# Performance work log

Measured on AMD Instinct MI355X. Metric: run time of the kernel, lower is better.

## Reference

```python
import jax, jax.numpy as jnp
import numpy as np

BATCH, SEQ, IN_DIM, HID = 256, 256, 128, 512
KMAX, MID, NCLS = 4, 256, 16  # maxout features, maxout/dense/highway width, output classes


def hard_sigmoid(x):
    return jnp.clip(0.2 * x + 0.5, 0.0, 1.0)


def setup_inputs() -> dict:
    key = jax.random.key(0)
    ks = jax.random.split(key, 20)
    s = 0.05
    d = {
        'x': jax.random.normal(ks[0], (BATCH, SEQ, IN_DIM), jnp.float32),
        'W_z': jax.random.normal(ks[1], (IN_DIM, HID), jnp.float32) * s,
        'W_r': jax.random.normal(ks[2], (IN_DIM, HID), jnp.float32) * s,
        'W_h': jax.random.normal(ks[3], (IN_DIM, HID), jnp.float32) * s,
        'U_z': jax.random.normal(ks[4], (HID, HID), jnp.float32) * s,
        'U_r': jax.random.normal(ks[5], (HID, HID), jnp.float32) * s,
        'U_h': jax.random.normal(ks[6], (HID, HID), jnp.float32) * s,
        'b_z': jax.random.normal(ks[7], (HID,), jnp.float32) * s,
        'b_r': jax.random.normal(ks[8], (HID,), jnp.float32) * s,
        'b_h': jax.random.normal(ks[9], (HID,), jnp.float32) * s,
        'mo_W': jax.random.normal(ks[10], (KMAX, HID, MID), jnp.float32) * s,
        'mo_b': jax.random.normal(ks[11], (KMAX, MID), jnp.float32) * s,
        'd1_W': jax.random.normal(ks[12], (MID, MID), jnp.float32) * s,
        'd1_b': jax.random.normal(ks[13], (MID,), jnp.float32) * s,
        'hw_W': jax.random.normal(ks[14], (MID, MID), jnp.float32) * s,
        'hw_b': jax.random.normal(ks[15], (MID,), jnp.float32) * s,
        'hw_Wc': jax.random.normal(ks[16], (MID, MID), jnp.float32) * s,
        'hw_bc': jax.random.normal(ks[17], (MID,), jnp.float32) * s,
        'd2_W': jax.random.normal(ks[18], (MID, NCLS), jnp.float32) * s,
        'd2_b': jax.random.normal(ks[19], (NCLS,), jnp.float32) * s,
    }
    return d


def reference(x, W_z, W_r, W_h, U_z, U_r, U_h, b_z, b_r, b_h,
              mo_W, mo_b, d1_W, d1_b, hw_W, hw_b, hw_Wc, hw_bc, d2_W, d2_b):
    # ---- Theano-convention GRU (reset applied before U_h matmul) ----
    # Precompute all input projections in one batched GEMM each: [B,S,H]
    xz = jnp.einsum('bsi,ih->bsh', x, W_z) + b_z
    xr = jnp.einsum('bsi,ih->bsh', x, W_r) + b_r
    xh = jnp.einsum('bsi,ih->bsh', x, W_h) + b_h

    def step(h, xs):
        xzt, xrt, xht = xs
        z = hard_sigmoid(xzt + h @ U_z)
        r = hard_sigmoid(xrt + h @ U_r)
        hh = jnp.tanh(xht + (r * h) @ U_h)
        h_new = z * h + (1.0 - z) * hh
        return h_new, None

    h0 = jnp.zeros((x.shape[0], U_z.shape[0]), x.dtype)
    # scan over time axis: move S to leading dim
    xs = (jnp.swapaxes(xz, 0, 1), jnp.swapaxes(xr, 0, 1), jnp.swapaxes(xh, 0, 1))
    h, _ = jax.lax.scan(step, h0, xs)

    # ---- Maxout dense ----
    h = jnp.max(jnp.einsum('bi,kio->bko', h, mo_W) + mo_b, axis=1)
    # ---- Dense (linear) ----
    h = h @ d1_W + d1_b
    # ---- Highway ----
    t = jax.nn.sigmoid(h @ hw_Wc + hw_bc)
    hh = jax.nn.relu(h @ hw_W + hw_b)
    h = t * hh + (1.0 - t) * h
    # ---- Dense + softmax ----
    logits = h @ d2_W + d2_b
    return jax.nn.softmax(logits, axis=-1)
```

## Files before the change

### kernel.cpp

```cpp
#include <hip/hip_runtime.h>
#include <hip/hip_bf16.h>
#include <math.h>

#define BATCH 256
#define SEQN  256
#define INDIM 128
#define HID   512
#define MID   256
#define NCLS  16

#define NG 8
#define RG 32
#define NS 16
#define SC 32

typedef _Float16 half8 __attribute__((ext_vector_type(8)));
typedef float    f32x4 __attribute__((ext_vector_type(4)));

__device__ __forceinline__ half8 cc_load16(const _Float16* p) {
    half8 r;
    asm volatile("global_load_dwordx4 %0, %1, off sc1" : "=&v"(r) : "v"(p));
    return r;
}
__device__ __forceinline__ void cc_wait() {
    asm volatile("s_waitcnt vmcnt(0)" ::: "memory");
    __builtin_amdgcn_sched_barrier(0);
}
__device__ __forceinline__ void cc_store16(_Float16* p, _Float16 v) {
    unsigned short u = __builtin_bit_cast(unsigned short, v);
    asm volatile("global_store_short %0, %1, off sc1" :: "v"(p), "v"(u) : "memory");
}

__global__ __launch_bounds__(256) void pack_wA(
    const float* __restrict__ Uz, const float* __restrict__ Ur,
    const float* __restrict__ Wz, const float* __restrict__ Wr,
    _Float16* __restrict__ out)
{
    int idx = blockIdx.x * 256 + threadIdx.x;
    int j = idx & 7, l = (idx >> 3) & 63;
    int fr = idx >> 9;
    int kt = fr % 20; int r2 = fr / 20;
    int nt4 = r2 & 3; int s = r2 >> 2;
    int k = kt * 32 + (l >> 4) * 8 + j;
    int col = s * SC + (nt4 & 1) * 16 + (l & 15);
    const float* U = (nt4 < 2) ? Uz : Ur;
    const float* W = (nt4 < 2) ? Wz : Wr;
    float v = (k < HID) ? U[k * HID + col] : W[(k - HID) * HID + col];
    out[idx] = (_Float16)v;
}

__global__ __launch_bounds__(256) void pack_wB(
    const float* __restrict__ Uh, const float* __restrict__ Wh,
    _Float16* __restrict__ out)
{
    int idx = blockIdx.x * 256 + threadIdx.x;
    int j = idx & 7, l = (idx >> 3) & 63;
    int fr = idx >> 9;
    int kt = fr % 20; int r2 = fr / 20;
    int nt2 = r2 & 1; int s = r2 >> 1;
    int k = kt * 32 + (l >> 4) * 8 + j;
    int col = s * SC + nt2 * 16 + (l & 15);
    float v = (k < HID) ? Uh[k * HID + col] : Wh[(k - HID) * HID + col];
    out[idx] = (_Float16)v;
}

__global__ __launch_bounds__(512) void gru_sync(
    const float* __restrict__ x, const _Float16* __restrict__ GWA,
    const _Float16* __restrict__ GWB,
    const float* __restrict__ bz, const float* __restrict__ br,
    const float* __restrict__ bh,
    _Float16* __restrict__ HF, _Float16* __restrict__ VF,
    unsigned int* __restrict__ cnt, float* __restrict__ hout)
{
    __shared__ _Float16 WA[4][20][64][8];
    __shared__ _Float16 WB[2][20][64][8];
    __shared__ float    HO[RG][SC];

    const int tid = threadIdx.x;
    const int w = tid >> 6, l = tid & 63;
    const int bid = blockIdx.x;
    const int g = bid & 7, s = bid >> 3;
    const int m = l & 15;
    const int crow0 = (l >> 4) * 4;

    const int mt  = w & 1;
    const int nt4 = w >> 1;
    const int nt2 = w >> 1;

    {
        const float4* srcA = (const float4*)&GWA[(size_t)s * (4 * 20 * 512)];
        float4* dstA = (float4*)&WA[0][0][0][0];
        for (int i = tid; i < 4 * 20 * 512 / 8; i += 512) dstA[i] = srcA[i];
        const float4* srcB = (const float4*)&GWB[(size_t)s * (2 * 20 * 512)];
        float4* dstB = (float4*)&WB[0][0][0][0];
        for (int i = tid; i < 2 * 20 * 512 / 8; i += 512) dstB[i] = srcB[i];
    }
    for (int i = tid; i < RG * SC; i += 512) ((float*)HO)[i] = 0.f;

    float biasA;
    {
        int col = s * SC + (nt4 & 1) * 16 + m;
        biasA = (nt4 < 2) ? bz[col] : br[col];
    }
    float biasB = 0.f;
    if (w < 4) biasB = bh[s * SC + nt2 * 16 + m];

    unsigned int* flag = &cnt[g * 32];
    __syncthreads();

    float zreg[4];

    for (int t = 0; t < SEQN; ++t) {
        half8 hfr[16];
        {
            const _Float16* hf = &HF[(size_t)(g * 2 + mt) * 16 * 512];
            #pragma unroll
            for (int kt = 0; kt < 16; ++kt)
                hfr[kt] = cc_load16(hf + kt * 512 + l * 8);
        }

        half8 xf[4];
        {
            const float* xp = &x[(((size_t)(g * RG + mt * 16 + m)) * SEQN + t) * INDIM + (l >> 4) * 8];
            #pragma unroll
            for (int kf = 0; kf < 4; ++kf) {
                float4 a0 = *(const float4*)(xp + kf * 32);
                float4 a1 = *(const float4*)(xp + kf * 32 + 4);
                half8 hx;
                hx[0] = (_Float16)a0.x; hx[1] = (_Float16)a0.y;
                hx[2] = (_Float16)a0.z; hx[3] = (_Float16)a0.w;
                hx[4] = (_Float16)a1.x; hx[5] = (_Float16)a1.y;
                hx[6] = (_Float16)a1.z; hx[7] = (_Float16)a1.w;
                xf[kf] = hx;
            }
        }
        cc_wait();

        {
            f32x4 acc = {0.f, 0.f, 0.f, 0.f};
            #pragma unroll
            for (int kt = 0; kt < 16; ++kt) {
                half8 bf = *(const half8*)&WA[nt4][kt][l][0];
                acc = __builtin_amdgcn_mfma_f32_16x16x32_f16(hfr[kt], bf, acc, 0, 0, 0);
            }
            #pragma unroll
            for (int kf = 0; kf < 4; ++kf) {
                half8 bf = *(const half8*)&WA[nt4][16 + kf][l][0];
                acc = __builtin_amdgcn_mfma_f32_16x16x32_f16(xf[kf], bf, acc, 0, 0, 0);
            }
            if (nt4 < 2) {
                #pragma unroll
                for (int ri = 0; ri < 4; ++ri) {
                    float pre = acc[ri] + biasA;
                    zreg[ri] = fminf(fmaxf(0.2f * pre + 0.5f, 0.f), 1.f);
                }
            } else {
                #pragma unroll
                for (int ri = 0; ri < 4; ++ri) {
                    float pre = acc[ri] + biasA;
                    float gr = fminf(fmaxf(0.2f * pre + 0.5f, 0.f), 1.f);
                    int rloc = mt * 16 + crow0 + ri;
                    int cs = (nt4 & 1) * 16 + m;
                    float vv = gr * HO[rloc][cs];
                    cc_store16(&VF[(((size_t)(g * 2 + mt) * 16 + s) * 64 +
                                    ((crow0 + ri) + 16 * (cs >> 3))) * 8 + (cs & 7)],
                               (_Float16)vv);
                }
            }
        }

        asm volatile("s_waitcnt vmcnt(0)" ::: "memory");
        __syncthreads();
        if (tid == 0) {
            __hip_atomic_fetch_add(flag, 1u, __ATOMIC_RELAXED, __HIP_MEMORY_SCOPE_AGENT);
            unsigned int tgt = (unsigned int)(2 * t + 1) * NS;
            while (__hip_atomic_load(flag, __ATOMIC_RELAXED, __HIP_MEMORY_SCOPE_AGENT) < tgt) {}
        }
        __syncthreads();

        if (w < 4) {
            half8 vfr[16];
            {
                const _Float16* vf = &VF[(size_t)(g * 2 + mt) * 16 * 512];
                #pragma unroll
                for (int kt = 0; kt < 16; ++kt)
                    vfr[kt] = cc_load16(vf + kt * 512 + l * 8);
            }
            cc_wait();

            f32x4 acc2 = {0.f, 0.f, 0.f, 0.f};
            #pragma unroll
            for (int kt = 0; kt < 16; ++kt) {
                half8 bf = *(const half8*)&WB[nt2][kt][l][0];
                acc2 = __builtin_amdgcn_mfma_f32_16x16x32_f16(vfr[kt], bf, acc2, 0, 0, 0);
            }
            #pragma unroll
            for (int kf = 0; kf < 4; ++kf) {
                half8 bf = *(const half8*)&WB[nt2][16 + kf][l][0];
                acc2 = __builtin_amdgcn_mfma_f32_16x16x32_f16(xf[kf], bf, acc2, 0, 0, 0);
            }
            #pragma unroll
            for (int ri = 0; ri < 4; ++ri) {
                float pre = acc2[ri] + biasB;
                float e  = __expf(2.f * pre);
                float hh = 1.f - 2.f / (e + 1.f);
                int rloc = mt * 16 + crow0 + ri;
                int cs = nt2 * 16 + m;
                float zz = zreg[ri];
                float ho = HO[rloc][cs];
                float hn = zz * ho + (1.f - zz) * hh;
                HO[rloc][cs] = hn;
                cc_store16(&HF[(((size_t)(g * 2 + mt) * 16 + s) * 64 +
                                ((crow0 + ri) + 16 * (cs >> 3))) * 8 + (cs & 7)],
                           (_Float16)hn);
            }
        }

        asm volatile("s_waitcnt vmcnt(0)" ::: "memory");
        __syncthreads();
        if (tid == 0) {
            __hip_atomic_fetch_add(flag, 1u, __ATOMIC_RELAXED, __HIP_MEMORY_SCOPE_AGENT);
            unsigned int tgt = (unsigned int)(2 * t + 2) * NS;
            while (__hip_atomic_load(flag, __ATOMIC_RELAXED, __HIP_MEMORY_SCOPE_AGENT) < tgt) {}
        }
        __syncthreads();
    }

    for (int i = tid; i < RG * SC; i += 512) {
        int r = i >> 5, c = i & 31;
        hout[(size_t)(g * RG + r) * HID + s * SC + c] = HO[r][c];
    }
}

__global__ __launch_bounds__(256) void maxout_k(
    const float* __restrict__ h, const float* __restrict__ moW,
    const float* __restrict__ mob, float* __restrict__ m)
{
    const int ot = blockIdx.x, bt = blockIdx.y;
    __shared__ float sA[32][33];
    __shared__ float sB[4][32][33];
    const int tid = threadIdx.x;
    const int tx = tid & 15, ty = tid >> 4;
    const int b0 = bt * 32, o0 = ot * 32;
    const int lr = tid >> 3, lk4 = (tid & 7) << 2;

    float acc[4][2][2];
    #pragma unroll
    for (int p = 0; p < 4; ++p)
        acc[p][0][0] = acc[p][0][1] = acc[p][1][0] = acc[p][1][1] = 0.f;

    for (int kt = 0; kt < 16; ++kt) {
        const int k0 = kt * 32;
        float4 a = *reinterpret_cast<const float4*>(&h[(b0 + lr) * HID + k0 + lk4]);
        float4 wv[4];
        #pragma unroll
        for (int p = 0; p < 4; ++p)
            wv[p] = *reinterpret_cast<const float4*>(&moW[((size_t)p * HID + k0 + lr) * MID + o0 + lk4]);
        __syncthreads();
        sA[lk4+0][lr] = a.x; sA[lk4+1][lr] = a.y; sA[lk4+2][lr] = a.z; sA[lk4+3][lr] = a.w;
        #pragma unroll
        for (int p = 0; p < 4; ++p) {
            sB[p][lr][lk4+0] = wv[p].x; sB[p][lr][lk4+1] = wv[p].y;
            sB[p][lr][lk4+2] = wv[p].z; sB[p][lr][lk4+3] = wv[p].w;
        }
        __syncthreads();
        #pragma unroll
        for (int kk = 0; kk < 32; ++kk) {
            float a0 = sA[kk][ty*2], a1 = sA[kk][ty*2+1];
            #pragma unroll
            for (int p = 0; p < 4; ++p) {
                float w0 = sB[p][kk][tx*2], w1 = sB[p][kk][tx*2+1];
                acc[p][0][0] += a0*w0; acc[p][0][1] += a0*w1;
                acc[p][1][0] += a1*w0; acc[p][1][1] += a1*w1;
            }
        }
    }

    #pragma unroll
    for (int q = 0; q < 2; ++q)
        #pragma unroll
        for (int c = 0; c < 2; ++c) {
            const int row = b0 + ty*2 + q, col = o0 + tx*2 + c;
            float best = -1e30f;
            #pragma unroll
            for (int p = 0; p < 4; ++p)
                best = fmaxf(best, acc[p][q][c] + mob[p * MID + col]);
            m[row * MID + col] = best;
        }
}

__global__ __launch_bounds__(256) void dense1_k(
    const float* __restrict__ m, const float* __restrict__ W,
    const float* __restrict__ b, float* __restrict__ a1)
{
    const int jt = blockIdx.x, bt = blockIdx.y;
    __shared__ float sA[32][33];
    __shared__ float sB[32][33];
    const int tid = threadIdx.x;
    const int tx = tid & 15, ty = tid >> 4;
    const int b0 = bt * 32, j0 = jt * 32;
    const int lr = tid >> 3, lk4 = (tid & 7) << 2;

    float acc[2][2] = {{0.f,0.f},{0.f,0.f}};

    for (int kt = 0; kt < 8; ++kt) {
        const int k0 = kt * 32;
        float4 a  = *reinterpret_cast<const float4*>(&m[(b0 + lr) * MID + k0 + lk4]);
        float4 bv = *reinterpret_cast<const float4*>(&W[(k0 + lr) * MID + j0 + lk4]);
        __syncthreads();
        sA[lk4+0][lr] = a.x; sA[lk4+1][lr] = a.y; sA[lk4+2][lr] = a.z; sA[lk4+3][lr] = a.w;
        sB[lr][lk4+0] = bv.x; sB[lr][lk4+1] = bv.y; sB[lr][lk4+2] = bv.z; sB[lr][lk4+3] = bv.w;
        __syncthreads();
        #pragma unroll
        for (int kk = 0; kk < 32; ++kk) {
            float a0 = sA[kk][ty*2], a1v = sA[kk][ty*2+1];
            float w0 = sB[kk][tx*2], w1 = sB[kk][tx*2+1];
            acc[0][0] += a0*w0; acc[0][1] += a0*w1;
            acc[1][0] += a1v*w0; acc[1][1] += a1v*w1;
        }
    }

    #pragma unroll
    for (int q = 0; q < 2; ++q)
        #pragma unroll
        for (int c = 0; c < 2; ++c) {
            const int row = b0 + ty*2 + q, col = j0 + tx*2 + c;
            a1[row * MID + col] = acc[q][c] + b[col];
        }
}

__global__ __launch_bounds__(256) void highway_k(
    const float* __restrict__ a1,
    const float* __restrict__ hwW, const float* __restrict__ hwb,
    const float* __restrict__ hwWc, const float* __restrict__ hwbc,
    float* __restrict__ h2)
{
    const int jt = blockIdx.x, bt = blockIdx.y;
    __shared__ float sA[32][33];
    __shared__ float sBh[32][33];
    __shared__ float sBc[32][33];
    const int tid = threadIdx.x;
    const int tx = tid & 15, ty = tid >> 4;
    const int b0 = bt * 32, j0 = jt * 32;
    const int lr = tid >> 3, lk4 = (tid & 7) << 2;

    float acch[2][2] = {{0.f,0.f},{0.f,0.f}};
    float accc[2][2] = {{0.f,0.f},{0.f,0.f}};

    for (int kt = 0; kt < 8; ++kt) {
        const int k0 = kt * 32;
        float4 a   = *reinterpret_cast<const float4*>(&a1[(b0 + lr) * MID + k0 + lk4]);
        float4 bh4 = *reinterpret_cast<const float4*>(&hwW[(k0 + lr) * MID + j0 + lk4]);
        float4 bc4 = *reinterpret_cast<const float4*>(&hwWc[(k0 + lr) * MID + j0 + lk4]);
        __syncthreads();
        sA[lk4+0][lr] = a.x; sA[lk4+1][lr] = a.y; sA[lk4+2][lr] = a.z; sA[lk4+3][lr] = a.w;
        sBh[lr][lk4+0] = bh4.x; sBh[lr][lk4+1] = bh4.y; sBh[lr][lk4+2] = bh4.z; sBh[lr][lk4+3] = bh4.w;
        sBc[lr][lk4+0] = bc4.x; sBc[lr][lk4+1] = bc4.y; sBc[lr][lk4+2] = bc4.z; sBc[lr][lk4+3] = bc4.w;
        __syncthreads();
        #pragma unroll
        for (int kk = 0; kk < 32; ++kk) {
            float a0 = sA[kk][ty*2], a1v = sA[kk][ty*2+1];
            float h0 = sBh[kk][tx*2], h1 = sBh[kk][tx*2+1];
            float c0 = sBc[kk][tx*2], c1 = sBc[kk][tx*2+1];
            acch[0][0] += a0*h0; acch[0][1] += a0*h1;
            acch[1][0] += a1v*h0; acch[1][1] += a1v*h1;
            accc[0][0] += a0*c0; accc[0][1] += a0*c1;
            accc[1][0] += a1v*c0; accc[1][1] += a1v*c1;
        }
    }

    #pragma unroll
    for (int q = 0; q < 2; ++q)
        #pragma unroll
        for (int c = 0; c < 2; ++c) {
            const int row = b0 + ty*2 + q, col = j0 + tx*2 + c;
            float tt = 1.f / (1.f + expf(-(accc[q][c] + hwbc[col])));
            float hp = fmaxf(acch[q][c] + hwb[col], 0.f);
            float av = a1[row * MID + col];
            h2[row * MID + col] = tt * hp + (1.f - tt) * av;
        }
}

__global__ __launch_bounds__(256) void d2_softmax(
    const float* __restrict__ h2, const float* __restrict__ W,
    const float* __restrict__ b, float* __restrict__ out)
{
    const int b0 = blockIdx.x * 16;
    const int r = threadIdx.x >> 4, c = threadIdx.x & 15;
    const int row = b0 + r;

    float acc = b[c];
    for (int i = 0; i < MID; ++i)
        acc += h2[row * MID + i] * W[i * NCLS + c];

    float mx = acc;
    #pragma unroll
    for (int off = 8; off; off >>= 1)
        mx = fmaxf(mx, __shfl_xor(mx, off, 16));
    float e = expf(acc - mx);
    float sm = e;
    #pragma unroll
    for (int off = 8; off; off >>= 1)
        sm += __shfl_xor(sm, off, 16);
    out[row * NCLS + c] = e / sm;
}

extern "C" void kernel_launch(void* const* d_in, const int* in_sizes, int n_in,
                              void* d_out, int out_size, void* d_ws, size_t ws_size,
                              hipStream_t stream) {
    (void)in_sizes; (void)n_in; (void)out_size; (void)ws_size;

    const float* x    = (const float*)d_in[0];
    const float* Wz   = (const float*)d_in[1];
    const float* Wr   = (const float*)d_in[2];
    const float* Wh   = (const float*)d_in[3];
    const float* Uz   = (const float*)d_in[4];
    const float* Ur   = (const float*)d_in[5];
    const float* Uh   = (const float*)d_in[6];
    const float* bz   = (const float*)d_in[7];
    const float* br   = (const float*)d_in[8];
    const float* bh   = (const float*)d_in[9];
    const float* moW  = (const float*)d_in[10];
    const float* mob  = (const float*)d_in[11];
    const float* d1W  = (const float*)d_in[12];
    const float* d1b  = (const float*)d_in[13];
    const float* hwW  = (const float*)d_in[14];
    const float* hwb  = (const float*)d_in[15];
    const float* hwWc = (const float*)d_in[16];
    const float* hwbc = (const float*)d_in[17];
    const float* d2W  = (const float*)d_in[18];
    const float* d2b  = (const float*)d_in[19];
    float* out = (float*)d_out;

    char* ws = (char*)d_ws;
    _Float16* GWA = (_Float16*)(ws + 0);
    _Float16* GWB = (_Float16*)(ws + 1310720);
    _Float16* HF  = (_Float16*)(ws + 1966080);
    _Float16* VF  = (_Float16*)(ws + 2228224);
    unsigned int* cnt = (unsigned int*)(ws + 2490368);
    float*    hbuf = (float*)(ws + 2491392);
    float*    mxb = (float*)(ws + 0);
    float*    a1b = (float*)(ws + 262144);
    float*    h2b = (float*)(ws + 524288);

    hipMemsetAsync(HF, 0, 262144, stream);
    hipMemsetAsync(cnt, 0, 1024, stream);

    pack_wA<<<2560, 256, 0, stream>>>(Uz, Ur, Wz, Wr, GWA);
    pack_wB<<<1280, 256, 0, stream>>>(Uh, Wh, GWB);

    gru_sync<<<128, 512, 0, stream>>>(x, GWA, GWB, bz, br, bh, HF, VF, cnt, hbuf);

    dim3 blk(256);
    maxout_k<<<dim3(8, 8), blk, 0, stream>>>(hbuf, moW, mob, mxb);
    dense1_k<<<dim3(8, 8), blk, 0, stream>>>(mxb, d1W, d1b, a1b);
    highway_k<<<dim3(8, 8), blk, 0, stream>>>(a1b, hwW, hwb, hwWc, hwbc, h2b);
    d2_softmax<<<16, blk, 0, stream>>>(h2b, d2W, d2b, out);
}
```

Baseline: 1.780 ms.

## Replace atomic counter barrier with per-block flag array and stage H/V via LDS

The single atomic-counter grid-group barrier becomes a flag array: each block writes its step number to its own slot, and one wavefront polls all 16 slots, exiting when every slot has reached the target. This removes atomic contention and serialisation on one counter. H and V state is no longer loaded redundantly by each wave. The block loads each once cooperatively into a shared LDS buffer (XB), and the MFMA operands are read from there. This adds extra __syncthreads and LDS traffic and relies on sc1 store/load ordering for correctness.

```diff
diff --git a/kernel.cpp b/kernel.cpp
--- a/kernel.cpp
+++ b/kernel.cpp
@@ -29,6 +29,24 @@
 __device__ __forceinline__ void cc_store16(_Float16* p, _Float16 v) {
     unsigned short u = __builtin_bit_cast(unsigned short, v);
     asm volatile("global_store_short %0, %1, off sc1" :: "v"(p), "v"(u) : "memory");
+}
+__device__ __forceinline__ void cc_store_u32(unsigned int* p, unsigned int v) {
+    asm volatile("global_store_dword %0, %1, off sc1" :: "v"(p), "v"(v) : "memory");
+}
+__device__ __forceinline__ unsigned int cc_load_u32(const unsigned int* p) {
+    unsigned int r;
+    asm volatile("global_load_dword %0, %1, off sc1\n\ts_waitcnt vmcnt(0)"
+                 : "=&v"(r) : "v"(p) : "memory");
+    return r;
+}
+
+__device__ __forceinline__ void group_barrier(unsigned int* base, int s, int l,
+                                              unsigned int tgt) {
+    if (l == 0) cc_store_u32(base + s, tgt);
+    unsigned int v;
+    do {
+        v = cc_load_u32(base + (l & 15));
+    } while (!__all((int)(v >= tgt)));
 }
 
 __global__ __launch_bounds__(256) void pack_wA(
@@ -70,11 +88,12 @@
     const float* __restrict__ bz, const float* __restrict__ br,
     const float* __restrict__ bh,
     _Float16* __restrict__ HF, _Float16* __restrict__ VF,
-    unsigned int* __restrict__ cnt, float* __restrict__ hout)
-{
-    __shared__ _Float16 WA[4][20][64][8];
-    __shared__ _Float16 WB[2][20][64][8];
-    __shared__ float    HO[RG][SC];
+    unsigned int* __restrict__ arr, float* __restrict__ hout)
+{
+    __shared__ __attribute__((aligned(16))) _Float16 WA[4][20][64][8];
+    __shared__ __attribute__((aligned(16))) _Float16 WB[2][20][64][8];
+    __shared__ __attribute__((aligned(16))) _Float16 XB[2][16][64][8];
+    __shared__ float HO[RG][SC];
 
     const int tid = threadIdx.x;
     const int w = tid >> 6, l = tid & 63;
@@ -105,48 +124,58 @@
     float biasB = 0.f;
     if (w < 4) biasB = bh[s * SC + nt2 * 16 + m];
 
-    unsigned int* flag = &cnt[g * 32];
+    unsigned int* abase = &arr[g * 64];
     __syncthreads();
 
     float zreg[4];
+    half8 xfr[4];
 
     for (int t = 0; t < SEQN; ++t) {
-        half8 hfr[16];
         {
-            const _Float16* hf = &HF[(size_t)(g * 2 + mt) * 16 * 512];
-            #pragma unroll
-            for (int kt = 0; kt < 16; ++kt)
-                hfr[kt] = cc_load16(hf + kt * 512 + l * 8);
-        }
-
-        half8 xf[4];
-        {
+            const _Float16* src = &HF[(size_t)g * (2 * 16 * 512)];
+            half8 tmp0 = cc_load16(src + (tid +    0) * 8);
+            half8 tmp1 = cc_load16(src + (tid +  512) * 8);
+            half8 tmp2 = cc_load16(src + (tid + 1024) * 8);
+            half8 tmp3 = cc_load16(src + (tid + 1536) * 8);
+
             const float* xp = &x[(((size_t)(g * RG + mt * 16 + m)) * SEQN + t) * INDIM + (l >> 4) * 8];
+            float4 xa[4], xb[4];
             #pragma unroll
             for (int kf = 0; kf < 4; ++kf) {
-                float4 a0 = *(const float4*)(xp + kf * 32);
-                float4 a1 = *(const float4*)(xp + kf * 32 + 4);
+                xa[kf] = *(const float4*)(xp + kf * 32);
+                xb[kf] = *(const float4*)(xp + kf * 32 + 4);
+            }
+            cc_wait();
+            half8* dst = (half8*)&XB[0][0][0][0];
+            dst[tid +    0] = tmp0;
+            dst[tid +  512] = tmp1;
+            dst[tid + 1024] = tmp2;
+            dst[tid + 1536] = tmp3;
+
+            #pragma unroll
+            for (int kf = 0; kf < 4; ++kf) {
                 half8 hx;
-                hx[0] = (_Float16)a0.x; hx[1] = (_Float16)a0.y;
-                hx[2] = (_Float16)a0.z; hx[3] = (_Float16)a0.w;
-                hx[4] = (_Float16)a1.x; hx[5] = (_Float16)a1.y;
-                hx[6] = (_Float16)a1.z; hx[7] = (_Float16)a1.w;
-                xf[kf] = hx;
-            }
-        }
-        cc_wait();
+                hx[0] = (_Float16)xa[kf].x; hx[1] = (_Float16)xa[kf].y;
+                hx[2] = (_Float16)xa[kf].z; hx[3] = (_Float16)xa[kf].w;
+                hx[4] = (_Float16)xb[kf].x; hx[5] = (_Float16)xb[kf].y;
+                hx[6] = (_Float16)xb[kf].z; hx[7] = (_Float16)xb[kf].w;
+                xfr[kf] = hx;
+            }
+        }
+        __syncthreads();
 
         {
             f32x4 acc = {0.f, 0.f, 0.f, 0.f};
             #pragma unroll
             for (int kt = 0; kt < 16; ++kt) {
+                half8 af = *(const half8*)&XB[mt][kt][l][0];
                 half8 bf = *(const half8*)&WA[nt4][kt][l][0];
-                acc = __builtin_amdgcn_mfma_f32_16x16x32_f16(hfr[kt], bf, acc, 0, 0, 0);
+                acc = __builtin_amdgcn_mfma_f32_16x16x32_f16(af, bf, acc, 0, 0, 0);
             }
             #pragma unroll
             for (int kf = 0; kf < 4; ++kf) {
                 half8 bf = *(const half8*)&WA[nt4][16 + kf][l][0];
-                acc = __builtin_amdgcn_mfma_f32_16x16x32_f16(xf[kf], bf, acc, 0, 0, 0);
+                acc = __builtin_amdgcn_mfma_f32_16x16x32_f16(xfr[kf], bf, acc, 0, 0, 0);
             }
             if (nt4 < 2) {
                 #pragma unroll
@@ -169,35 +198,37 @@
             }
         }
 
-        asm volatile("s_waitcnt vmcnt(0)" ::: "memory");
-        __syncthreads();
-        if (tid == 0) {
-            __hip_atomic_fetch_add(flag, 1u, __ATOMIC_RELAXED, __HIP_MEMORY_SCOPE_AGENT);
-            unsigned int tgt = (unsigned int)(2 * t + 1) * NS;
-            while (__hip_atomic_load(flag, __ATOMIC_RELAXED, __HIP_MEMORY_SCOPE_AGENT) < tgt) {}
+        __syncthreads();
+        if (w == 0) group_barrier(abase, s, l, (unsigned int)(2 * t + 1));
+        __syncthreads();
+
+        {
+            const _Float16* src = &VF[(size_t)g * (2 * 16 * 512)];
+            half8 tmp0 = cc_load16(src + (tid +    0) * 8);
+            half8 tmp1 = cc_load16(src + (tid +  512) * 8);
+            half8 tmp2 = cc_load16(src + (tid + 1024) * 8);
+            half8 tmp3 = cc_load16(src + (tid + 1536) * 8);
+            cc_wait();
+            half8* dst = (half8*)&XB[0][0][0][0];
+            dst[tid +    0] = tmp0;
+            dst[tid +  512] = tmp1;
+            dst[tid + 1024] = tmp2;
+            dst[tid + 1536] = tmp3;
         }
         __syncthreads();
 
         if (w < 4) {
-            half8 vfr[16];
-            {
-                const _Float16* vf = &VF[(size_t)(g * 2 + mt) * 16 * 512];
-                #pragma unroll
-                for (int kt = 0; kt < 16; ++kt)
-                    vfr[kt] = cc_load16(vf + kt * 512 + l * 8);
-            }
-            cc_wait();
-
             f32x4 acc2 = {0.f, 0.f, 0.f, 0.f};
             #pragma unroll
             for (int kt = 0; kt < 16; ++kt) {
+                half8 af = *(const half8*)&XB[mt][kt][l][0];
                 half8 bf = *(const half8*)&WB[nt2][kt][l][0];
-                acc2 = __builtin_amdgcn_mfma_f32_16x16x32_f16(vfr[kt], bf, acc2, 0, 0, 0);
+                acc2 = __builtin_amdgcn_mfma_f32_16x16x32_f16(af, bf, acc2, 0, 0, 0);
             }
             #pragma unroll
             for (int kf = 0; kf < 4; ++kf) {
                 half8 bf = *(const half8*)&WB[nt2][16 + kf][l][0];
-                acc2 = __builtin_amdgcn_mfma_f32_16x16x32_f16(xf[kf], bf, acc2, 0, 0, 0);
+                acc2 = __builtin_amdgcn_mfma_f32_16x16x32_f16(xfr[kf], bf, acc2, 0, 0, 0);
             }
             #pragma unroll
             for (int ri = 0; ri < 4; ++ri) {
@@ -216,13 +247,8 @@
             }
         }
 
-        asm volatile("s_waitcnt vmcnt(0)" ::: "memory");
-        __syncthreads();
-        if (tid == 0) {
-            __hip_atomic_fetch_add(flag, 1u, __ATOMIC_RELAXED, __HIP_MEMORY_SCOPE_AGENT);
-            unsigned int tgt = (unsigned int)(2 * t + 2) * NS;
-            while (__hip_atomic_load(flag, __ATOMIC_RELAXED, __HIP_MEMORY_SCOPE_AGENT) < tgt) {}
-        }
+        __syncthreads();
+        if (w == 0) group_barrier(abase, s, l, (unsigned int)(2 * t + 2));
         __syncthreads();
     }
 
@@ -437,19 +463,19 @@
     _Float16* GWB = (_Float16*)(ws + 1310720);
     _Float16* HF  = (_Float16*)(ws + 1966080);
     _Float16* VF  = (_Float16*)(ws + 2228224);
-    unsigned int* cnt = (unsigned int*)(ws + 2490368);
-    float*    hbuf = (float*)(ws + 2491392);
+    unsigned int* arr = (unsigned int*)(ws + 2490368);
+    float*    hbuf = (float*)(ws + 2492416);
     float*    mxb = (float*)(ws + 0);
     float*    a1b = (float*)(ws + 262144);
     float*    h2b = (float*)(ws + 524288);
 
     hipMemsetAsync(HF, 0, 262144, stream);
-    hipMemsetAsync(cnt, 0, 1024, stream);
+    hipMemsetAsync(arr, 0, 2048, stream);
 
     pack_wA<<<2560, 256, 0, stream>>>(Uz, Ur, Wz, Wr, GWA);
     pack_wB<<<1280, 256, 0, stream>>>(Uh, Wh, GWB);
 
-    gru_sync<<<128, 512, 0, stream>>>(x, GWA, GWB, bz, br, bh, HF, VF, cnt, hbuf);
+    gru_sync<<<128, 512, 0, stream>>>(x, GWA, GWB, bz, br, bh, HF, VF, arr, hbuf);
 
     dim3 blk(256);
     maxout_k<<<dim3(8, 8), blk, 0, stream>>>(hbuf, moW, mob, mxb);
```

Result: slower. 1.922 ms (+8.0%).
